# Kernel optimization log

Measured on AMD Instinct MI355X. Metric: run time of the kernel, lower is better.

The kernel has to match this reference:

```python
import jax, jax.numpy as jnp
import numpy as np

NUM_CLASSES = 1000  # label vocabulary size (matches fill_max for label)
B = 16384
D_IN = 1024   # image_embedding
D_OUT = 256   # projection_dim


def setup_inputs() -> dict:
    key = jax.random.key(0)
    k = jax.random.split(key, 6)
    x = jax.random.normal(k[0], (B, D_IN), dtype=jnp.float32)
    label = jax.random.randint(k[1], (B,), 0, NUM_CLASSES, dtype=jnp.int64)
    scale = 1.0 / np.sqrt(D_IN)
    W1_w = jax.random.normal(k[2], (D_OUT, D_IN), dtype=jnp.float32) * scale
    W1_b = jax.random.normal(k[3], (D_OUT,), dtype=jnp.float32) * scale
    W2_w = jax.random.normal(k[4], (D_OUT, D_IN), dtype=jnp.float32) * scale
    W2_b = jax.random.normal(k[5], (D_OUT,), dtype=jnp.float32) * scale
    return {"x": x, "label": label, "W1_w": W1_w, "W1_b": W1_b,
            "W2_w": W2_w, "W2_b": W2_b}


def reference(x, label, W1_w, W1_b, W2_w, W2_b):
    # Leave-one-group-out mean, vectorized via segment sums.
    # Original: for each i, mean of x[label != label_i] (detached); zeros if none.
    b = x.shape[0]
    xd = jax.lax.stop_gradient(x)  # .detach() in the torch code
    label_sum = jax.ops.segment_sum(xd, label, num_segments=NUM_CLASSES)          # [C, D_IN]
    label_cnt = jax.ops.segment_sum(jnp.ones((b,), dtype=x.dtype), label,
                                    num_segments=NUM_CLASSES)                     # [C]
    total_sum = xd.sum(axis=0)                                                    # [D_IN]
    other_sum = total_sum[None, :] - label_sum[label]                             # [B, D_IN]
    other_cnt = jnp.asarray(b, x.dtype) - label_cnt[label]                        # [B]
    calculate_mean = jnp.where(other_cnt[:, None] > 0,
                               other_sum / jnp.maximum(other_cnt, 1)[:, None],
                               jnp.zeros((), x.dtype))                            # [B, D_IN]
    # W1(x) + W2(calculate_mean)  (torch Linear: y = x @ W.T + b)
    return x @ W1_w.T + W1_b + calculate_mean @ W2_w.T + W2_b
```

## Files before the change

kernel.cpp:

```cpp
#include <hip/hip_runtime.h>

constexpr int B      = 16384;
constexpr int D_IN   = 1024;
constexpr int D_OUT  = 256;
constexpr int NCLS   = 1000;

constexpr size_t OFF_XB  = 0;
constexpr size_t OFF_WB  = OFF_XB + (size_t)B * D_IN * 2;
constexpr size_t OFF_Y1  = OFF_WB + (size_t)512 * D_IN * 2;
constexpr size_t OFF_V   = OFF_Y1 + (size_t)B * D_OUT * 4;
constexpr size_t OFF_U   = OFF_V  + (size_t)1024 * D_OUT * 4;
constexpr size_t OFF_CNT = OFF_U  + 4096;

typedef short bf16x8 __attribute__((ext_vector_type(8)));
typedef float f32x4  __attribute__((ext_vector_type(4)));

__device__ __forceinline__ unsigned short f2bf(float f) {
    unsigned int u = __float_as_uint(f);
    return (unsigned short)((u + 0x7FFFu + ((u >> 16) & 1u)) >> 16);
}

__device__ __forceinline__ void cvt8(const float4& a, const float4& b, unsigned short* dst) {
    union { unsigned short u[8]; bf16x8 v; } r;
    r.u[0] = f2bf(a.x); r.u[1] = f2bf(a.y); r.u[2] = f2bf(a.z); r.u[3] = f2bf(a.w);
    r.u[4] = f2bf(b.x); r.u[5] = f2bf(b.y); r.u[6] = f2bf(b.z); r.u[7] = f2bf(b.w);
    *(bf16x8*)dst = r.v;
}

__device__ __forceinline__ void async16(const unsigned short* g, unsigned short* l) {
    __builtin_amdgcn_global_load_lds(
        (const __attribute__((address_space(1))) void*)g,
        (__attribute__((address_space(3))) void*)l,
        16, 0, 0);
}

constexpr int XCVT_BLKS = 4096;
constexpr int WCVT_BLKS = 128;
constexpr int VZ_BLKS   = 64;
__global__ __launch_bounds__(256)
void prep_kernel(const float* __restrict__ x,
                 const float* __restrict__ W1, const float* __restrict__ W2,
                 const int* __restrict__ label,
                 unsigned short* __restrict__ xb, unsigned short* __restrict__ Wb,
                 float* __restrict__ V, float* __restrict__ U, int* __restrict__ cnt) {
    const int blk = blockIdx.x, tid = threadIdx.x;
    if (blk == 0) {
        __shared__ int h[1024];
#pragma unroll
        for (int q = 0; q < 4; ++q) h[q * 256 + tid] = 0;
        __syncthreads();
        for (int base = 0; base < 64; base += 16) {
            int lv[16];
#pragma unroll
            for (int u = 0; u < 16; ++u) lv[u] = label[(base + u) * 256 + tid];
#pragma unroll
            for (int u = 0; u < 16; ++u) atomicAdd(&h[lv[u]], 1);
        }
        __syncthreads();
#pragma unroll
        for (int q = 0; q < 4; ++q) cnt[q * 256 + tid] = h[q * 256 + tid];
    } else if (blk <= XCVT_BLKS) {
        size_t lin = (size_t)(blk - 1) * 256 + tid;
        const float* src = x + lin * 16;
        float4 a0 = *(const float4*)(src);
        float4 a1 = *(const float4*)(src + 4);
        float4 a2 = *(const float4*)(src + 8);
        float4 a3 = *(const float4*)(src + 12);
        cvt8(a0, a1, xb + lin * 16);
        cvt8(a2, a3, xb + lin * 16 + 8);
    } else if (blk <= XCVT_BLKS + WCVT_BLKS) {
        int lin = (blk - 1 - XCVT_BLKS) * 256 + tid;
        int i = lin * 16;
        const float* src = (i < D_OUT * D_IN) ? (W1 + i) : (W2 + (i - D_OUT * D_IN));
        float4 a0 = *(const float4*)(src);
        float4 a1 = *(const float4*)(src + 4);
        float4 a2 = *(const float4*)(src + 8);
        float4 a3 = *(const float4*)(src + 12);
        cvt8(a0, a1, Wb + i);
        cvt8(a2, a3, Wb + i + 8);
    } else {
        int lb = blk - 1 - XCVT_BLKS - WCVT_BLKS;
        int base = (lb * 256 + tid) * 16;
#pragma unroll
        for (int q = 0; q < 4; ++q)
            *(float4*)(V + base + q * 4) = float4{0.f, 0.f, 0.f, 0.f};
        if (lb == 0 && tid < 64)
            *(float4*)(U + tid * 4) = float4{0.f, 0.f, 0.f, 0.f};
    }
}

__global__ __launch_bounds__(256)
void gemm_kernel(const unsigned short* __restrict__ xb,
                 const unsigned short* __restrict__ Wb,
                 const int* __restrict__ label,
                 float* __restrict__ y1,
                 float* __restrict__ V, float* __restrict__ U) {
    __shared__ unsigned short As[128][64];
    __shared__ unsigned short Bs[128][64];

    const int tid  = threadIdx.x;
    const int bid  = blockIdx.x;
    const int xcd   = bid & 7;
    const int local = bid >> 3;
    const int bx = xcd * 16 + (local & 15);
    const int by = local >> 4;
    const int bm = bx * 128;
    const int bn = by * 128;

    const int wave = tid >> 6, lane = tid & 63;
    const int quad = lane >> 4, l16 = lane & 15;
    const int wm = (wave >> 1) * 64;
    const int wn = (wave & 1) * 64;
    const int sx = l16 & 7;

    const unsigned short* aps[4];
    const unsigned short* bps[4];
#pragma unroll
    for (int rr = 0; rr < 4; ++rr) {
        int dd = rr * 256 + tid;
        int r = dd >> 3, sl = dd & 7;
        int sc = sl ^ (r & 7);
        aps[rr] = xb + (size_t)(bm + r) * D_IN + sc * 8;
        bps[rr] = Wb + (size_t)(bn + r) * D_IN + sc * 8;
    }

    f32x4 acc[4][4] = {};

    for (int k0 = 0; k0 < D_IN; k0 += 64) {
        __syncthreads();
#pragma unroll
        for (int rr = 0; rr < 4; ++rr)
            async16(aps[rr] + k0, &As[0][0] + rr * 2048 + wave * 512);
#pragma unroll
        for (int rr = 0; rr < 4; ++rr)
            async16(bps[rr] + k0, &Bs[0][0] + rr * 2048 + wave * 512);
        __syncthreads();

#pragma unroll
        for (int ks = 0; ks < 2; ++ks) {
            const int s = ks * 4 + quad;
            bf16x8 af[4], bfr[4];
#pragma unroll
            for (int i = 0; i < 4; ++i)
                af[i] = *(const bf16x8*)&As[wm + i * 16 + l16][((s ^ sx) * 8)];
#pragma unroll
            for (int j = 0; j < 4; ++j)
                bfr[j] = *(const bf16x8*)&Bs[wn + j * 16 + l16][((s ^ sx) * 8)];
#pragma unroll
            for (int i = 0; i < 4; ++i)
#pragma unroll
                for (int j = 0; j < 4; ++j)
                    acc[i][j] = __builtin_amdgcn_mfma_f32_16x16x32_bf16(af[i], bfr[j], acc[i][j], 0, 0, 0);
        }
    }

    if (by < 2) {
#pragma unroll
        for (int j = 0; j < 4; ++j) {
            const int n = bn + wn + j * 16 + l16;
#pragma unroll
            for (int i = 0; i < 4; ++i)
#pragma unroll
                for (int r = 0; r < 4; ++r) {
                    const int m = bm + wm + i * 16 + quad * 4 + r;
                    y1[(size_t)m * D_OUT + n] = acc[i][j][r];
                }
        }
    } else {
        int lab[4][4];
#pragma unroll
        for (int i = 0; i < 4; ++i)
#pragma unroll
            for (int r = 0; r < 4; ++r)
                lab[i][r] = label[bm + wm + i * 16 + quad * 4 + r] * D_OUT;

        const int nb = bn - 256;
#pragma unroll
        for (int j = 0; j < 4; ++j) {
            const int n = nb + wn + j * 16 + l16;
            float cs = 0.f;
#pragma unroll
            for (int i = 0; i < 4; ++i)
#pragma unroll
                for (int r = 0; r < 4; ++r) {
                    float v = acc[i][j][r];
                    cs += v;
                    atomicAdd(&V[lab[i][r] + n], v);
                }
            cs += __shfl_xor(cs, 16);
            cs += __shfl_xor(cs, 32);
            if (quad == 0) atomicAdd(&U[n], cs);
        }
    }
}

__global__ __launch_bounds__(256)
void epi_kernel(const float* __restrict__ y1, const float* __restrict__ V,
                const float* __restrict__ U,
                const float* __restrict__ b1, const float* __restrict__ b2,
                const int* __restrict__ cnt, const int* __restrict__ label,
                float* __restrict__ out) {
    const int tid = threadIdx.x;
    const int row = blockIdx.x * 64 + (tid >> 2);
    const int lab = label[row];
    const float inv = 1.0f / (float)(B - cnt[lab]);
    const float* yp = y1 + (size_t)row * D_OUT;
    const float* vp = V  + (size_t)lab * D_OUT;
    float* op = out + (size_t)row * D_OUT;
    const int c0 = (tid & 3) * 4;
#pragma unroll
    for (int it = 0; it < 16; ++it) {
        const int c = c0 + it * 16;
        float4 y = *(const float4*)(yp + c);
        float4 v = *(const float4*)(vp + c);
        float4 u = *(const float4*)(U + c);
        float4 a1 = *(const float4*)(b1 + c);
        float4 a2 = *(const float4*)(b2 + c);
        float4 o;
        o.x = y.x + a1.x + a2.x + (u.x - v.x) * inv;
        o.y = y.y + a1.y + a2.y + (u.y - v.y) * inv;
        o.z = y.z + a1.z + a2.z + (u.z - v.z) * inv;
        o.w = y.w + a1.w + a2.w + (u.w - v.w) * inv;
        *(float4*)(op + c) = o;
    }
}

extern "C" void kernel_launch(void* const* d_in, const int* in_sizes, int n_in,
                              void* d_out, int out_size, void* d_ws, size_t ws_size,
                              hipStream_t stream) {
    const float* x    = (const float*)d_in[0];
    const int*   lab  = (const int*)d_in[1];
    const float* W1_w = (const float*)d_in[2];
    const float* W1_b = (const float*)d_in[3];
    const float* W2_w = (const float*)d_in[4];
    const float* W2_b = (const float*)d_in[5];
    float* out = (float*)d_out;

    char* ws = (char*)d_ws;
    unsigned short* xb = (unsigned short*)(ws + OFF_XB);
    unsigned short* Wb = (unsigned short*)(ws + OFF_WB);
    float* y1 = (float*)(ws + OFF_Y1);
    float* V  = (float*)(ws + OFF_V);
    float* U  = (float*)(ws + OFF_U);
    int*   cnt = (int*)(ws + OFF_CNT);

    prep_kernel<<<1 + XCVT_BLKS + WCVT_BLKS + VZ_BLKS, 256, 0, stream>>>(
        x, W1_w, W2_w, lab, xb, Wb, V, U, cnt);
    gemm_kernel<<<512, 256, 0, stream>>>(xb, Wb, lab, y1, V, U);
    epi_kernel<<<B / 64, 256, 0, stream>>>(y1, V, U, W1_b, W2_b, cnt, lab, out);
}
```

Before: 160.1 us.

## Fuse x fp32-to-bf16 conversion into GEMM with double-buffered LDS pipeline

Stops converting x to bf16 in a separate pass through a workspace buffer. The GEMM now loads fp32 x directly, converts it in registers with packed bf16 conversion, and writes it to LDS. LDS is double-buffered, with the next tile's x loads and W async copies overlapped with the MFMA work on the current tile. This removes a 64MB read plus a 32MB write and read round trip, at the cost of more registers, 64KB of LDS per block, and GEMM loads that now pull fp32 data, twice the bytes.

```diff
diff --git a/kernel.cpp b/kernel.cpp
--- a/kernel.cpp
+++ b/kernel.cpp
@@ -5,8 +5,7 @@
 constexpr int D_OUT  = 256;
 constexpr int NCLS   = 1000;
 
-constexpr size_t OFF_XB  = 0;
-constexpr size_t OFF_WB  = OFF_XB + (size_t)B * D_IN * 2;
+constexpr size_t OFF_WB  = 0;
 constexpr size_t OFF_Y1  = OFF_WB + (size_t)512 * D_IN * 2;
 constexpr size_t OFF_V   = OFF_Y1 + (size_t)B * D_OUT * 4;
 constexpr size_t OFF_U   = OFF_V  + (size_t)1024 * D_OUT * 4;
@@ -27,6 +26,12 @@
     *(bf16x8*)dst = r.v;
 }
 
+__device__ __forceinline__ unsigned int cvtpk(float lo, float hi) {
+    unsigned int r;
+    asm volatile("v_cvt_pk_bf16_f32 %0, %1, %2" : "=v"(r) : "v"(lo), "v"(hi));
+    return r;
+}
+
 __device__ __forceinline__ void async16(const unsigned short* g, unsigned short* l) {
     __builtin_amdgcn_global_load_lds(
         (const __attribute__((address_space(1))) void*)g,
@@ -34,14 +39,10 @@
         16, 0, 0);
 }
 
-constexpr int XCVT_BLKS = 4096;
-constexpr int WCVT_BLKS = 128;
-constexpr int VZ_BLKS   = 64;
 __global__ __launch_bounds__(256)
-void prep_kernel(const float* __restrict__ x,
-                 const float* __restrict__ W1, const float* __restrict__ W2,
+void prep_kernel(const float* __restrict__ W1, const float* __restrict__ W2,
                  const int* __restrict__ label,
-                 unsigned short* __restrict__ xb, unsigned short* __restrict__ Wb,
+                 unsigned short* __restrict__ Wb,
                  float* __restrict__ V, float* __restrict__ U, int* __restrict__ cnt) {
     const int blk = blockIdx.x, tid = threadIdx.x;
     if (blk == 0) {
@@ -59,17 +60,8 @@
         __syncthreads();
 #pragma unroll
         for (int q = 0; q < 4; ++q) cnt[q * 256 + tid] = h[q * 256 + tid];
-    } else if (blk <= XCVT_BLKS) {
-        size_t lin = (size_t)(blk - 1) * 256 + tid;
-        const float* src = x + lin * 16;
-        float4 a0 = *(const float4*)(src);
-        float4 a1 = *(const float4*)(src + 4);
-        float4 a2 = *(const float4*)(src + 8);
-        float4 a3 = *(const float4*)(src + 12);
-        cvt8(a0, a1, xb + lin * 16);
-        cvt8(a2, a3, xb + lin * 16 + 8);
-    } else if (blk <= XCVT_BLKS + WCVT_BLKS) {
-        int lin = (blk - 1 - XCVT_BLKS) * 256 + tid;
+    } else if (blk <= 128) {
+        int lin = (blk - 1) * 256 + tid;
         int i = lin * 16;
         const float* src = (i < D_OUT * D_IN) ? (W1 + i) : (W2 + (i - D_OUT * D_IN));
         float4 a0 = *(const float4*)(src);
@@ -79,7 +71,7 @@
         cvt8(a0, a1, Wb + i);
         cvt8(a2, a3, Wb + i + 8);
     } else {
-        int lb = blk - 1 - XCVT_BLKS - WCVT_BLKS;
+        int lb = blk - 129;
         int base = (lb * 256 + tid) * 16;
 #pragma unroll
         for (int q = 0; q < 4; ++q)
@@ -89,14 +81,14 @@
     }
 }
 
-__global__ __launch_bounds__(256)
-void gemm_kernel(const unsigned short* __restrict__ xb,
+__global__ __launch_bounds__(256, 2)
+void gemm_kernel(const float* __restrict__ x,
                  const unsigned short* __restrict__ Wb,
                  const int* __restrict__ label,
                  float* __restrict__ y1,
                  float* __restrict__ V, float* __restrict__ U) {
-    __shared__ unsigned short As[128][64];
-    __shared__ unsigned short Bs[128][64];
+    __shared__ unsigned short As[2][128][64];
+    __shared__ unsigned short Bs[2][128][64];
 
     const int tid  = threadIdx.x;
     const int bid  = blockIdx.x;
@@ -113,28 +105,67 @@
     const int wn = (wave & 1) * 64;
     const int sx = l16 & 7;
 
-    const unsigned short* aps[4];
-    const unsigned short* bps[4];
+    const float* xps[4];
+    int adst[4];
 #pragma unroll
     for (int rr = 0; rr < 4; ++rr) {
         int dd = rr * 256 + tid;
         int r = dd >> 3, sl = dd & 7;
         int sc = sl ^ (r & 7);
-        aps[rr] = xb + (size_t)(bm + r) * D_IN + sc * 8;
+        xps[rr] = x + (size_t)(bm + r) * D_IN + sc * 8;
+        adst[rr] = dd * 8;
+    }
+    const unsigned short* bps[4];
+#pragma unroll
+    for (int rr = 0; rr < 4; ++rr) {
+        int dd = rr * 256 + tid;
+        int r = dd >> 3, sl = dd & 7;
+        int sc = sl ^ (r & 7);
         bps[rr] = Wb + (size_t)(bn + r) * D_IN + sc * 8;
     }
 
     f32x4 acc[4][4] = {};
-
-    for (int k0 = 0; k0 < D_IN; k0 += 64) {
-        __syncthreads();
-#pragma unroll
-        for (int rr = 0; rr < 4; ++rr)
-            async16(aps[rr] + k0, &As[0][0] + rr * 2048 + wave * 512);
-#pragma unroll
-        for (int rr = 0; rr < 4; ++rr)
-            async16(bps[rr] + k0, &Bs[0][0] + rr * 2048 + wave * 512);
-        __syncthreads();
+    float4 a0[4], a1[4];
+
+#pragma unroll
+    for (int rr = 0; rr < 4; ++rr) {
+        a0[rr] = *(const float4*)(xps[rr]);
+        a1[rr] = *(const float4*)(xps[rr] + 4);
+    }
+#pragma unroll
+    for (int rr = 0; rr < 4; ++rr)
+        async16(bps[rr], &Bs[0][0][0] + rr * 2048 + wave * 512);
+#pragma unroll
+    for (int rr = 0; rr < 4; ++rr) {
+        union { unsigned int w[4]; bf16x8 v; } p;
+        p.w[0] = cvtpk(a0[rr].x, a0[rr].y);
+        p.w[1] = cvtpk(a0[rr].z, a0[rr].w);
+        p.w[2] = cvtpk(a1[rr].x, a1[rr].y);
+        p.w[3] = cvtpk(a1[rr].z, a1[rr].w);
+        *(bf16x8*)(&As[0][0][0] + adst[rr]) = p.v;
+    }
+
+    for (int t = 0; t < 16; ++t) {
+        const int cur = t & 1;
+        const int k1 = (t + 1) * 64;
+        if (t < 15) {
+#pragma unroll
+            for (int rr = 0; rr < 4; ++rr) {
+                a0[rr] = *(const float4*)(xps[rr] + k1);
+                a1[rr] = *(const float4*)(xps[rr] + k1 + 4);
+            }
+            asm volatile("s_waitcnt vmcnt(8)" ::: "memory");
+        } else {
+            asm volatile("s_waitcnt vmcnt(0)" ::: "memory");
+        }
+        asm volatile("s_waitcnt lgkmcnt(0)" ::: "memory");
+        __builtin_amdgcn_s_barrier();
+        __builtin_amdgcn_sched_barrier(0);
+        if (t < 15) {
+#pragma unroll
+            for (int rr = 0; rr < 4; ++rr)
+                async16(bps[rr] + k1, &Bs[cur ^ 1][0][0] + rr * 2048 + wave * 512);
+        }
 
 #pragma unroll
         for (int ks = 0; ks < 2; ++ks) {
@@ -142,15 +173,27 @@
             bf16x8 af[4], bfr[4];
 #pragma unroll
             for (int i = 0; i < 4; ++i)
-                af[i] = *(const bf16x8*)&As[wm + i * 16 + l16][((s ^ sx) * 8)];
+                af[i] = *(const bf16x8*)&As[cur][wm + i * 16 + l16][((s ^ sx) * 8)];
 #pragma unroll
             for (int j = 0; j < 4; ++j)
-                bfr[j] = *(const bf16x8*)&Bs[wn + j * 16 + l16][((s ^ sx) * 8)];
+                bfr[j] = *(const bf16x8*)&Bs[cur][wn + j * 16 + l16][((s ^ sx) * 8)];
 #pragma unroll
             for (int i = 0; i < 4; ++i)
 #pragma unroll
                 for (int j = 0; j < 4; ++j)
                     acc[i][j] = __builtin_amdgcn_mfma_f32_16x16x32_bf16(af[i], bfr[j], acc[i][j], 0, 0, 0);
+        }
+
+        if (t < 15) {
+#pragma unroll
+            for (int rr = 0; rr < 4; ++rr) {
+                union { unsigned int w[4]; bf16x8 v; } p;
+                p.w[0] = cvtpk(a0[rr].x, a0[rr].y);
+                p.w[1] = cvtpk(a0[rr].z, a0[rr].w);
+                p.w[2] = cvtpk(a1[rr].x, a1[rr].y);
+                p.w[3] = cvtpk(a1[rr].z, a1[rr].w);
+                *(bf16x8*)(&As[cur ^ 1][0][0] + adst[rr]) = p.v;
+            }
         }
     }
 
@@ -237,15 +280,13 @@
     float* out = (float*)d_out;
 
     char* ws = (char*)d_ws;
-    unsigned short* xb = (unsigned short*)(ws + OFF_XB);
     unsigned short* Wb = (unsigned short*)(ws + OFF_WB);
     float* y1 = (float*)(ws + OFF_Y1);
     float* V  = (float*)(ws + OFF_V);
     float* U  = (float*)(ws + OFF_U);
     int*   cnt = (int*)(ws + OFF_CNT);
 
-    prep_kernel<<<1 + XCVT_BLKS + WCVT_BLKS + VZ_BLKS, 256, 0, stream>>>(
-        x, W1_w, W2_w, lab, xb, Wb, V, U, cnt);
-    gemm_kernel<<<512, 256, 0, stream>>>(xb, Wb, lab, y1, V, U);
+    prep_kernel<<<193, 256, 0, stream>>>(W1_w, W2_w, lab, Wb, V, U, cnt);
+    gemm_kernel<<<512, 256, 0, stream>>>(x, Wb, lab, y1, V, U);
     epi_kernel<<<B / 64, 256, 0, stream>>>(y1, V, U, W1_b, W2_b, cnt, lab, out);
 }
```

Measured after the change: 148.8 us. 1.08x faster.
